# Kernel optimization log

Hardware: AMD Instinct MI355X
Metric: run time of the kernel (lower is better)

Reference implementation:

```python
import jax, jax.numpy as jnp
import numpy as np

B = 8192
D = 1024
NUM_CLASSES = 128
EPS = 1e-8  # torch F.cosine_similarity default eps


def setup_inputs() -> dict:
    key = jax.random.key(0)
    k1, k2, k3 = jax.random.split(key, 3)
    label_tensor = jax.random.randint(k1, (B,), 0, NUM_CLASSES, dtype=jnp.int64 if jax.config.jax_enable_x64 else jnp.int32)
    feature_a = jax.random.normal(k2, (B, D), dtype=jnp.float32)
    feature_b = jax.random.normal(k3, (B, D), dtype=jnp.float32)
    return {"label_tensor": label_tensor, "feature_a": feature_a, "feature_b": feature_b}


def reference(label_tensor, feature_a, feature_b):
    # Pairwise cosine similarity: cos_score[i, k] = cos(a_i, b_k), shape [B, B]
    dots = feature_a @ feature_b.T  # [B, B]
    na = jnp.linalg.norm(feature_a, axis=1)  # [B]
    nb = jnp.linalg.norm(feature_b, axis=1)  # [B]
    cos_score = dots / jnp.maximum(na[:, None] * nb[None, :], EPS)
    # Row-softmax (torch softmax dim=1 on the [B, B] matrix)
    logp = jax.nn.log_softmax(cos_score, axis=1)
    # Label-equality mask: positives for row i are all j with same label
    mask = (label_tensor[:, None] == label_tensor[None, :]).astype(cos_score.dtype)  # [B, B]
    per_row = -(mask * logp).sum(axis=1) / mask.sum(axis=1)  # diagonal guarantees >=1 positive
    loss = per_row.mean()
    return loss, cos_score
```

## Files before the change

### kernel.cpp

```cpp
#include <hip/hip_runtime.h>
#include <hip/hip_bf16.h>

#define NB 8192
#define ND 1024

typedef __bf16 bf16x8 __attribute__((ext_vector_type(8)));
typedef float  f32x4  __attribute__((ext_vector_type(4)));

__device__ inline void gload_lds16(const void* g, void* l) {
    __builtin_amdgcn_global_load_lds(
        (const __attribute__((address_space(1))) unsigned int*)g,
        (__attribute__((address_space(3))) unsigned int*)l,
        16, 0, 0);
}

__device__ inline unsigned short f2bf(float x) {
    unsigned int u = __float_as_uint(x);
    return (unsigned short)((u + 0x7fffu + ((u >> 16) & 1u)) >> 16);
}

#define BARRIER() asm volatile("s_barrier" ::: "memory")
#define VMCNT0()  asm volatile("s_waitcnt vmcnt(0)" ::: "memory")
#define LGKM0()   do { asm volatile("s_waitcnt lgkmcnt(0)" ::: "memory"); \
                       __builtin_amdgcn_sched_barrier(0); } while (0)

__global__ __launch_bounds__(256) void prep_kernel(
    const float* __restrict__ A, const float* __restrict__ Bm,
    unsigned short* __restrict__ wa, unsigned short* __restrict__ wb,
    float* __restrict__ na, float* __restrict__ nb)
{
    int b = blockIdx.x;
    int wid = threadIdx.x >> 6, lane = threadIdx.x & 63;
    const float* src; unsigned short* dst; float* nrm; int row;
    if (b < 2048) { src = A;  dst = wa; nrm = na; row = b * 4 + wid; }
    else          { src = Bm; dst = wb; nrm = nb; row = (b - 2048) * 4 + wid; }

    const float*    rp = src + (size_t)row * ND;
    unsigned short* wp = dst + (size_t)row * ND;

    float ss = 0.f;
#pragma unroll
    for (int t = 0; t < 4; ++t) {
        int c = lane * 4 + t * 256;
        float4 v = *reinterpret_cast<const float4*>(rp + c);
        ss += v.x * v.x + v.y * v.y + v.z * v.z + v.w * v.w;
        ushort4 u;
        u.x = f2bf(v.x); u.y = f2bf(v.y); u.z = f2bf(v.z); u.w = f2bf(v.w);
        *reinterpret_cast<ushort4*>(wp + c) = u;
    }
#pragma unroll
    for (int off = 32; off; off >>= 1) ss += __shfl_xor(ss, off);
    if (lane == 0) nrm[row] = sqrtf(ss);
}

__global__ __launch_bounds__(256) void hist_kernel(
    const int* __restrict__ labels, int* __restrict__ hist)
{
    __shared__ int h[128];
    int tid = threadIdx.x;
    if (tid < 128) h[tid] = 0;
    __syncthreads();
    for (int i = tid; i < NB; i += 256) atomicAdd(&h[labels[i]], 1);
    __syncthreads();
    if (tid < 128) hist[tid] = h[tid];
}

__global__ __launch_bounds__(512, 2) void gemm_cos(
    const unsigned short* __restrict__ wa, const unsigned short* __restrict__ wb,
    const float* __restrict__ na, const float* __restrict__ nb,
    const int* __restrict__ labels,
    float* __restrict__ C, float* __restrict__ pe, float* __restrict__ pm)
{
    __shared__ unsigned short lds[65536];

    const int bid = blockIdx.x;
    const int tm  = (bid & 7) * 4 + ((bid >> 3) & 3);
    const int tn  = bid >> 5;

    const int tid  = threadIdx.x;
    const int lane = tid & 63;
    const int wid  = tid >> 6;
    const int wr   = wid >> 2, wc = wid & 3;
    const int l15  = lane & 15, lg = lane >> 4;

    const int m0 = tm * 256, n0 = tn * 256;

    const int srow6 = tid >> 3;
    const int sgr   = (tid & 7) ^ (srow6 & 7);
    const unsigned short* pA = wa + (size_t)(m0 + srow6) * ND + sgr * 8;
    const unsigned short* pB = wb + (size_t)(n0 + srow6) * ND + sgr * 8;
    const int stW = wid * 512;
    const int ND64 = 64 * ND;

    const int swz0  = ((((l15 >> 2) & 1) << 2) | (lg ^ (l15 & 3))) * 8;
    const int baseA = (wr * 128 + l15) * 64 + swz0;
    const int baseB = 16384 + (wc * 64 + l15) * 64 + swz0;

    f32x4 acc[8][4];
#pragma unroll
    for (int i = 0; i < 8; ++i)
#pragma unroll
        for (int j = 0; j < 4; ++j) acc[i][j] = (f32x4){0.f, 0.f, 0.f, 0.f};

    bf16x8 bq[4];

#define STG4(P, DST) do { \
    gload_lds16((P),            &lds[(DST) + 0 * 4096 + stW]); \
    gload_lds16((P) +     ND64, &lds[(DST) + 1 * 4096 + stW]); \
    gload_lds16((P) + 2 * ND64, &lds[(DST) + 2 * 4096 + stW]); \
    gload_lds16((P) + 3 * ND64, &lds[(DST) + 3 * 4096 + stW]); } while (0)

#define PH(BUFB, KS, MH, RB, GATE, ...) { \
    if (RB) { _Pragma("unroll") \
        for (int n_ = 0; n_ < 4; ++n_) \
            bq[n_] = *reinterpret_cast<const bf16x8*>( \
                &lds[(BUFB) + ((baseB + n_ * 1024) ^ ((KS) * 32))]); } \
    bf16x8 af[4]; \
    _Pragma("unroll") \
    for (int m_ = 0; m_ < 4; ++m_) \
        af[m_] = *reinterpret_cast<const bf16x8*>( \
            &lds[(BUFB) + ((baseA + ((MH) * 4 + m_) * 1024) ^ ((KS) * 32))]); \
    __VA_ARGS__; \
    BARRIER(); \
    LGKM0(); \
    __builtin_amdgcn_s_setprio(1); \
    _Pragma("unroll") \
    for (int m_ = 0; m_ < 4; ++m_) \
        _Pragma("unroll") \
        for (int n_ = 0; n_ < 4; ++n_) \
            acc[(MH) * 4 + m_][n_] = __builtin_amdgcn_mfma_f32_16x16x32_bf16( \
                af[m_], bq[n_], acc[(MH) * 4 + m_][n_], 0, 0, 0); \
    __builtin_amdgcn_s_setprio(0); \
    if (GATE) VMCNT0(); \
    BARRIER(); }

    STG4(pA, 0); STG4(pB, 16384);
    VMCNT0();
    BARRIER();

    for (int j = 0; j < 8; ++j) {
        const unsigned short* s1 = pA + (2 * j + 1) * 64;
        const unsigned short* t1 = pB + (2 * j + 1) * 64;
        PH(0, 0, 0, 1, 0, STG4(s1, 32768))
        PH(0, 0, 1, 0, 0, STG4(t1, 32768 + 16384))
        PH(0, 1, 0, 1, 0, (void)0)
        PH(0, 1, 1, 0, 1, (void)0)
        if (j < 7) {
            const unsigned short* s2 = pA + (2 * j + 2) * 64;
            const unsigned short* t2 = pB + (2 * j + 2) * 64;
            PH(32768, 0, 0, 1, 0, STG4(s2, 0))
            PH(32768, 0, 1, 0, 0, STG4(t2, 16384))
            PH(32768, 1, 0, 1, 0, (void)0)
            PH(32768, 1, 1, 0, 1, (void)0)
        } else {
            PH(32768, 0, 0, 1, 0, (void)0)
            PH(32768, 0, 1, 0, 0, (void)0)
            PH(32768, 1, 0, 1, 0, (void)0)
            PH(32768, 1, 1, 0, 1, (void)0)
        }
    }

#undef PH
#undef STG4

    __syncthreads();
    float* pl = reinterpret_cast<float*>(lds);

    float nbv[4]; int labc[4];
#pragma unroll
    for (int n = 0; n < 4; ++n) {
        int c = n0 + wc * 64 + n * 16 + l15;
        nbv[n] = nb[c]; labc[n] = labels[c];
    }

#pragma unroll
    for (int m = 0; m < 8; ++m) {
#pragma unroll
        for (int jj = 0; jj < 4; ++jj) {
            int rl = wr * 128 + m * 16 + lg * 4 + jj;
            int r  = m0 + rl;
            float nav = na[r]; int labr = labels[r];
            float es = 0.f, ms = 0.f;
#pragma unroll
            for (int n = 0; n < 4; ++n) {
                int c = n0 + wc * 64 + n * 16 + l15;
                float v = acc[m][n][jj] / fmaxf(nav * nbv[n], 1e-8f);
                C[(size_t)r * NB + c] = v;
                es += __expf(v);
                ms += (labc[n] == labr) ? v : 0.f;
            }
#pragma unroll
            for (int off = 1; off < 16; off <<= 1) {
                es += __shfl_xor(es, off);
                ms += __shfl_xor(ms, off);
            }
            if (l15 == 0) {
                int o = (rl * 4 + wc) * 2;
                pl[o] = es; pl[o + 1] = ms;
            }
        }
    }
    __syncthreads();
    if (tid < 256) {
        float es = 0.f, ms = 0.f;
#pragma unroll
        for (int w = 0; w < 4; ++w) {
            es += pl[(tid * 4 + w) * 2];
            ms += pl[(tid * 4 + w) * 2 + 1];
        }
        int grow = m0 + tid;
        pe[tn * NB + grow] = es;
        pm[tn * NB + grow] = ms;
    }
}

__global__ __launch_bounds__(256) void loss_final(
    const float* __restrict__ pe, const float* __restrict__ pm,
    const int* __restrict__ labels, const int* __restrict__ hist,
    float* __restrict__ per_row)
{
    int row = blockIdx.x * 256 + threadIdx.x;
    float es = 0.f, ms = 0.f;
#pragma unroll
    for (int t = 0; t < 32; ++t) {
        es += pe[t * NB + row];
        ms += pm[t * NB + row];
    }
    per_row[row] = logf(es) - ms / (float)hist[labels[row]];
}

__global__ __launch_bounds__(256) void finalize(
    const float* __restrict__ per_row, float* __restrict__ out)
{
    __shared__ float sm[256];
    float s = 0.f;
    for (int i = threadIdx.x; i < NB; i += 256) s += per_row[i];
    sm[threadIdx.x] = s;
    __syncthreads();
    for (int k = 128; k; k >>= 1) {
        if (threadIdx.x < k) sm[threadIdx.x] += sm[threadIdx.x + k];
        __syncthreads();
    }
    if (threadIdx.x == 0) out[0] = sm[0] * (1.0f / (float)NB);
}

extern "C" void kernel_launch(void* const* d_in, const int* in_sizes, int n_in,
                              void* d_out, int out_size, void* d_ws, size_t ws_size,
                              hipStream_t stream) {
    const int*   labels = (const int*)d_in[0];
    const float* A      = (const float*)d_in[1];
    const float* Bm     = (const float*)d_in[2];
    float* out = (float*)d_out;

    char* ws = (char*)d_ws;
    unsigned short* wa = (unsigned short*)(ws);
    unsigned short* wb = (unsigned short*)(ws + 16777216);
    float* na      = (float*)(ws + 33554432);
    float* nb      = (float*)(ws + 33554432 + 32768);
    float* per_row = (float*)(ws + 33554432 + 65536);
    int*   hist    = (int*)  (ws + 33554432 + 98304);
    float* pe      = (float*)(ws + 33554432 + 131072);
    float* pm      = (float*)(ws + 33554432 + 131072 + 1048576);

    float* cosm = out + 1;

    prep_kernel<<<4096, 256, 0, stream>>>(A, Bm, wa, wb, na, nb);
    hist_kernel<<<1,    256, 0, stream>>>(labels, hist);
    gemm_cos   <<<1024, 512, 0, stream>>>(wa, wb, na, nb, labels, cosm, pe, pm);
    loss_final <<<32,   256, 0, stream>>>(pe, pm, labels, hist, per_row);
    finalize   <<<1,    256, 0, stream>>>(per_row, out);
}
```

Baseline: 248.9 us.

## Spread next-tile global-to-LDS loads across all four MFMA phases with partial waits

Changes the GEMM main loop so that prefetching the next K-tile is split into four two-load chunks, one per MFMA phase, instead of two four-load bursts in the first two phases. It replaces the full vmcnt(0) wait at the end of each tile with vmcnt(2) waits in selected phases, so loads can stay in flight across barriers. The loop is rewritten as a fully unrolled 16-step loop with precomputed XOR-swizzled LDS base offsets. The intent is smoother memory traffic and less stalling on outstanding loads. The risk is that the partial waits get the ordering wrong and read LDS before it is filled, and the larger unrolled body adds code size and register pressure.

```diff
diff --git a/kernel.cpp b/kernel.cpp
--- a/kernel.cpp
+++ b/kernel.cpp
@@ -20,6 +20,7 @@
 }
 
 #define BARRIER() asm volatile("s_barrier" ::: "memory")
+#define VMCNT2()  asm volatile("s_waitcnt vmcnt(2)" ::: "memory")
 #define VMCNT0()  asm volatile("s_waitcnt vmcnt(0)" ::: "memory")
 #define LGKM0()   do { asm volatile("s_waitcnt lgkmcnt(0)" ::: "memory"); \
                        __builtin_amdgcn_sched_barrier(0); } while (0)
@@ -87,14 +88,18 @@
 
     const int srow6 = tid >> 3;
     const int sgr   = (tid & 7) ^ (srow6 & 7);
-    const unsigned short* pA = wa + (size_t)(m0 + srow6) * ND + sgr * 8;
-    const unsigned short* pB = wb + (size_t)(n0 + srow6) * ND + sgr * 8;
-    const int stW = wid * 512;
-    const int ND64 = 64 * ND;
+    const unsigned short* pA0 = wa + (size_t)(m0 + srow6) * ND + sgr * 8;
+    const unsigned short* pA1 = pA0 + 64 * ND;
+    const unsigned short* pB0 = wb + (size_t)(n0 + srow6) * ND + sgr * 8;
+    const unsigned short* pB1 = pB0 + 64 * ND;
+    const int stW  = wid * 512;
+    const int ND128 = 128 * ND;
 
     const int swz0  = ((((l15 >> 2) & 1) << 2) | (lg ^ (l15 & 3))) * 8;
-    const int baseA = (wr * 128 + l15) * 64 + swz0;
-    const int baseB = 16384 + (wc * 64 + l15) * 64 + swz0;
+    const int bA0 = (wr * 128 + l15) * 64 + swz0;
+    const int bA1 = bA0 ^ 32;
+    const int bB0 = 16384 + (wc * 64 + l15) * 64 + swz0;
+    const int bB1 = bB0 ^ 32;
 
     f32x4 acc[8][4];
 #pragma unroll
@@ -104,23 +109,20 @@
 
     bf16x8 bq[4];
 
-#define STG4(P, DST) do { \
-    gload_lds16((P),            &lds[(DST) + 0 * 4096 + stW]); \
-    gload_lds16((P) +     ND64, &lds[(DST) + 1 * 4096 + stW]); \
-    gload_lds16((P) + 2 * ND64, &lds[(DST) + 2 * 4096 + stW]); \
-    gload_lds16((P) + 3 * ND64, &lds[(DST) + 3 * 4096 + stW]); } while (0)
-
-#define PH(BUFB, KS, MH, RB, GATE, ...) { \
+#define STG(P, DOFF) do { \
+    gload_lds16((P),          &lds[(DOFF) + stW]); \
+    gload_lds16((P) + ND128,  &lds[(DOFF) + 8192 + stW]); } while (0)
+
+#define PH(CB, BA, BB, MH, RB, STGX, GATE) { \
     if (RB) { _Pragma("unroll") \
         for (int n_ = 0; n_ < 4; ++n_) \
-            bq[n_] = *reinterpret_cast<const bf16x8*>( \
-                &lds[(BUFB) + ((baseB + n_ * 1024) ^ ((KS) * 32))]); } \
+            bq[n_] = *reinterpret_cast<const bf16x8*>(&lds[(CB) + (BB) + n_ * 1024]); } \
     bf16x8 af[4]; \
     _Pragma("unroll") \
     for (int m_ = 0; m_ < 4; ++m_) \
         af[m_] = *reinterpret_cast<const bf16x8*>( \
-            &lds[(BUFB) + ((baseA + ((MH) * 4 + m_) * 1024) ^ ((KS) * 32))]); \
-    __VA_ARGS__; \
+            &lds[(CB) + (BA) + ((MH) * 4 + m_) * 1024]); \
+    STGX; \
     BARRIER(); \
     LGKM0(); \
     __builtin_amdgcn_s_setprio(1); \
@@ -131,37 +133,34 @@
             acc[(MH) * 4 + m_][n_] = __builtin_amdgcn_mfma_f32_16x16x32_bf16( \
                 af[m_], bq[n_], acc[(MH) * 4 + m_][n_], 0, 0, 0); \
     __builtin_amdgcn_s_setprio(0); \
-    if (GATE) VMCNT0(); \
+    GATE; \
     BARRIER(); }
 
-    STG4(pA, 0); STG4(pB, 16384);
+    STG(pA0, 0);  STG(pA1, 4096);
+    STG(pB0, 16384); STG(pB1, 16384 + 4096);
     VMCNT0();
     BARRIER();
 
-    for (int j = 0; j < 8; ++j) {
-        const unsigned short* s1 = pA + (2 * j + 1) * 64;
-        const unsigned short* t1 = pB + (2 * j + 1) * 64;
-        PH(0, 0, 0, 1, 0, STG4(s1, 32768))
-        PH(0, 0, 1, 0, 0, STG4(t1, 32768 + 16384))
-        PH(0, 1, 0, 1, 0, (void)0)
-        PH(0, 1, 1, 0, 1, (void)0)
-        if (j < 7) {
-            const unsigned short* s2 = pA + (2 * j + 2) * 64;
-            const unsigned short* t2 = pB + (2 * j + 2) * 64;
-            PH(32768, 0, 0, 1, 0, STG4(s2, 0))
-            PH(32768, 0, 1, 0, 0, STG4(t2, 16384))
-            PH(32768, 1, 0, 1, 0, (void)0)
-            PH(32768, 1, 1, 0, 1, (void)0)
+#pragma unroll
+    for (int t = 0; t < 16; ++t) {
+        const int cb = (t & 1) * 32768;
+        const int sb = cb ^ 32768;
+        const int ko = (t + 1) * 64;
+        if (t < 15) {
+            PH(cb, bA0, bB0, 0, 1, STG(pB0 + ko, sb + 16384),        VMCNT2())
+            PH(cb, bA0, bB0, 1, 0, STG(pB1 + ko, sb + 16384 + 4096), (void)0)
+            PH(cb, bA1, bB1, 0, 1, STG(pA0 + ko, sb),                (void)0)
+            PH(cb, bA1, bB1, 1, 0, STG(pA1 + ko, sb + 4096),         VMCNT2())
         } else {
-            PH(32768, 0, 0, 1, 0, (void)0)
-            PH(32768, 0, 1, 0, 0, (void)0)
-            PH(32768, 1, 0, 1, 0, (void)0)
-            PH(32768, 1, 1, 0, 1, (void)0)
+            PH(cb, bA0, bB0, 0, 1, (void)0, VMCNT0())
+            PH(cb, bA0, bB0, 1, 0, (void)0, (void)0)
+            PH(cb, bA1, bB1, 0, 1, (void)0, (void)0)
+            PH(cb, bA1, bB1, 1, 0, (void)0, (void)0)
         }
     }
 
 #undef PH
-#undef STG4
+#undef STG
 
     __syncthreads();
     float* pl = reinterpret_cast<float*>(lds);
```

After: 243.5 us. -2.2%, faster.
